# Optimization experiments

Hardware: AMD Instinct MI355X
Metric: run time of the kernel (lower is better)

## Reference

```python
import jax, jax.numpy as jnp
import numpy as np

N = 20000          # num nodes
E = 320000         # num edges
D = 128            # in_channels (= out_channels)
H = 8              # num_heads
HD = D // H        # head_dim = 16


def setup_inputs() -> dict:
    key = jax.random.key(0)
    ks = jax.random.split(key, 10)
    s = 0.05
    return {
        "x": jax.random.normal(ks[0], (N, D), jnp.float32),
        "edges": jax.random.randint(ks[1], (E, 2), 0, N, jnp.int64),
        "Wp": jax.random.normal(ks[2], (D, D), jnp.float32) * s,
        "bp": jax.random.normal(ks[3], (D,), jnp.float32) * s,
        "Wm": jax.random.normal(ks[4], (D, D), jnp.float32) * s,
        "bm": jax.random.normal(ks[5], (D,), jnp.float32) * s,
        "W1": jax.random.normal(ks[6], (D, 2 * D), jnp.float32) * s,
        "b1": jax.random.normal(ks[7], (D,), jnp.float32) * s,
        "W2": jax.random.normal(ks[8], (D, D), jnp.float32) * s,
        "b2": jax.random.normal(ks[9], (D,), jnp.float32) * s,
    }


def reference(x, edges, Wp, bp, Wm, bm, W1, b1, W2, b2):
    # edges: [E,2] -> row (src), col (dst)
    row, col = edges[:, 0], edges[:, 1]
    src = x[row]                       # [E, D] gather
    dst = x[col]                       # [E, D] gather
    # shared preprocess Linear for q, k, v (key == value == dst features)
    q = src @ Wp.T + bp                # [E, D]
    kv = dst @ Wp.T + bp               # [E, D]
    # view(E, -1, H, HD).transpose(1,2) with seq_len 1 -> effectively [E, H, HD]
    q = q.reshape(E, H, HD)
    k = kv.reshape(E, H, HD)
    v = k
    # original attention() misreads axes: contracts over HEAD axis, scale 1/sqrt(H),
    # softmax over the head_dim axis -> scores [E, HD, HD]
    scores = jnp.einsum("ehn,ehm->enm", q, k) / jnp.sqrt(jnp.float32(H))
    prob = jax.nn.softmax(scores, axis=-1)          # [E, HD, HD]
    out = jnp.einsum("enm,ehm->ehn", prob, v)       # [E, H, HD]
    # view(E, HD*H, 1) then 1x1 Conv1d merge == Linear
    msg = out.reshape(E, H * HD) @ Wm.T + bm        # [E, D]
    # scatter-sum aggregate by destination node (empty -> 0, matches torch loop)
    agg = jax.ops.segment_sum(msg, col, num_segments=N)  # [N, D]
    h = jnp.concatenate([x, agg], axis=1)           # [N, 2D]
    h = jax.nn.relu(h @ W1.T + b1)
    return h @ W2.T + b2                            # [N, D]
```

## Files before the change

kernel.cpp:

```cpp
#include <hip/hip_runtime.h>

#define NN 20000
#define EE 320000
#define DEGCAP 64

typedef _Float16 half4_t __attribute__((ext_vector_type(4)));
typedef float f32x4 __attribute__((ext_vector_type(4)));

#define MFMA16F16 __builtin_amdgcn_mfma_f32_16x16x16f16

__global__ __launch_bounds__(256) void setup_kernel(
    int4* __restrict__ countv,
    const float* __restrict__ Wp, const float* __restrict__ Wm,
    const float* __restrict__ W1, const float* __restrict__ W2,
    _Float16* __restrict__ wpt, _Float16* __restrict__ wmt,
    _Float16* __restrict__ w1t, _Float16* __restrict__ w2t) {
  const int b = blockIdx.x, t = threadIdx.x;
  if (b < 20) {
    countv[b * 256 + t] = int4{0, 0, 0, 0};
    return;
  }
  const int tid = (b - 20) * 256 + t;
  const float* W; _Float16* dst; int K, l;
  if (tid < 16384)      { W = Wp; dst = wpt; K = 128; l = tid; }
  else if (tid < 32768) { W = Wm; dst = wmt; K = 128; l = tid - 16384; }
  else if (tid < 65536) { W = W1; dst = w1t; K = 256; l = tid - 32768; }
  else                  { W = W2; dst = w2t; K = 128; l = tid - 65536; }
  const int j = l & 3, n = (l >> 2) & 15, g = (l >> 6) & 3;
  const int ot = (l >> 8) & 7, kt = l >> 11;
  const int k = kt * 16 + 4 * g + j, o = ot * 16 + n;
  dst[l] = (_Float16)W[o * K + k];
}

__global__ __launch_bounds__(256) void bin_proj_kernel(
    const int* __restrict__ edges, int* __restrict__ count,
    int* __restrict__ srow,
    const float* __restrict__ x, const _Float16* __restrict__ wpt,
    const float* __restrict__ bp, _Float16* __restrict__ ph) {
  const int b = blockIdx.x, t = threadIdx.x;
  if (b < 1250) {
    const int e = b * 256 + t;
    const int row = edges[2 * e];
    const int col = edges[2 * e + 1];
    const int slot = atomicAdd(&count[col], 1);
    if (slot < DEGCAP) srow[col * DEGCAP + slot] = row;
    return;
  }
  const int wv = __builtin_amdgcn_readfirstlane(t >> 6), lane = t & 63;
  const int n = lane & 15, g = lane >> 4;
  const int rb = (b - 1250) * 16;
  const int arow = rb + n;

  half4_t a[8];
#pragma unroll
  for (int kt = 0; kt < 8; ++kt) {
    const float4 xv = *(const float4*)&x[(size_t)arow * 128 + kt * 16 + 4 * g];
    half4_t h; h[0] = (_Float16)xv.x; h[1] = (_Float16)xv.y;
    h[2] = (_Float16)xv.z; h[3] = (_Float16)xv.w;
    a[kt] = h;
  }
  const f32x4 zero = {0.f, 0.f, 0.f, 0.f};
#pragma unroll
  for (int oi = 0; oi < 2; ++oi) {
    const int ot = wv * 2 + oi;
    f32x4 acc = zero;
#pragma unroll
    for (int kt = 0; kt < 8; ++kt) {
      const half4_t bb = *(const half4_t*)&wpt[(((kt * 8 + ot) * 4 + g) << 6) + n * 4];
      acc = MFMA16F16(a[kt], bb, acc, 0, 0, 0);
    }
    const float bpv = bp[ot * 16 + n];
#pragma unroll
    for (int r = 0; r < 4; ++r) {
      const int nrow = rb + 4 * g + r;
      ph[(size_t)nrow * 128 + n * 8 + ot] = (_Float16)(acc[r] + bpv);
    }
  }
}

__global__ __launch_bounds__(512) void edge_node_kernel(
    const _Float16* __restrict__ ph, const int* __restrict__ count,
    const int* __restrict__ srow,
    const float* __restrict__ x,
    const _Float16* __restrict__ wmt, const float* __restrict__ bm,
    const _Float16* __restrict__ w1t, const float* __restrict__ b1,
    const _Float16* __restrict__ w2t, const float* __restrict__ b2,
    float* __restrict__ out) {
  __shared__ _Float16 agl[16 * 132];
  __shared__ _Float16 mh[16 * 132];
  __shared__ _Float16 hh[16 * 132];
  const int t = threadIdx.x;
  const int wv = __builtin_amdgcn_readfirstlane(t >> 6);
  const int lane = t & 63;
  const int n = lane & 15, g = lane >> 4;
  const int rb = blockIdx.x * 16;
  const f32x4 zero = {0.f, 0.f, 0.f, 0.f};
  const float c2 = 0.5101268320290106f;
  const int laneoff = n * 8 + 4 * g;

  const int col0 = rb + wv * 2, col1 = col0 + 1;
  const _Float16* __restrict__ pc0 = ph + ((unsigned)col0 << 7);
  const _Float16* __restrict__ pc1 = ph + ((unsigned)col1 << 7);
  half4_t ka0{}, ka1{};
  if (g < 2) {
    ka0 = *(const half4_t*)&pc0[n * 8 + 4 * g];
    ka1 = *(const half4_t*)&pc1[n * 8 + 4 * g];
  }
  half4_t a20{}, a21{};
  if (n < 8) {
#pragma unroll
    for (int j = 0; j < 4; ++j) {
      a20[j] = pc0[(4 * g + j) * 8 + n];
      a21[j] = pc1[(4 * g + j) * 8 + n];
    }
  }
  const int d0raw = count[col0], d1raw = count[col1];
  const int deg0 = (d0raw < DEGCAP) ? d0raw : DEGCAP;
  const int deg1 = (d1raw < DEGCAP) ? d1raw : DEGCAP;
  const int dm0 = (deg0 > 0) ? deg0 - 1 : 0;
  const int dm1 = (deg1 > 0) ? deg1 - 1 : 0;
  const int maxdeg = (deg0 > deg1) ? deg0 : deg1;
  const int slots0 = srow[col0 * DEGCAP + lane];
  const int slots1 = srow[col1 * DEGCAP + lane];
  f32x4 psum0 = zero, psum1 = zero;

#define GATHER(DST, SLOTS, DM, IDX)                                          \
  {                                                                          \
    const int ii_ = ((IDX) < (DM)) ? (IDX) : (DM);                           \
    int row_ = __builtin_amdgcn_readlane(SLOTS, ii_);                        \
    row_ = ((unsigned)row_ < NN) ? row_ : 0;        \
    DST = *(const half4_t*)&ph[((unsigned)row_ << 7) + laneoff];             \
  }
#define PROC(Q, KA, PSUM, IDX, DEG)                                          \
  {                                                                          \
    f32x4 s_ = MFMA16F16(KA, Q, zero, 0, 0, 0);                              \
    const float p0_ = __builtin_amdgcn_exp2f((float)s_[0] * c2);             \
    const float p1_ = __builtin_amdgcn_exp2f((float)s_[1] * c2);             \
    const float p2_ = __builtin_amdgcn_exp2f((float)s_[2] * c2);             \
    const float p3_ = __builtin_amdgcn_exp2f((float)s_[3] * c2);             \
    float sum_ = (p0_ + p1_) + (p2_ + p3_);                                  \
    sum_ += __shfl_xor(sum_, 16, 64);                                        \
    sum_ += __shfl_xor(sum_, 32, 64);                                        \
    const float inv_ =                                                       \
        ((IDX) < (DEG)) ? __builtin_amdgcn_rcpf(sum_) : 0.f;                 \
    PSUM[0] = fmaf(p0_, inv_, PSUM[0]);                                      \
    PSUM[1] = fmaf(p1_, inv_, PSUM[1]);                                      \
    PSUM[2] = fmaf(p2_, inv_, PSUM[2]);                                      \
    PSUM[3] = fmaf(p3_, inv_, PSUM[3]);                                      \
  }

  if (maxdeg > 0) {
    half4_t qA0, qA1, qB0, qB1;
    GATHER(qA0, slots0, dm0, 0) GATHER(qB0, slots1, dm1, 0)
    GATHER(qA1, slots0, dm0, 1) GATHER(qB1, slots1, dm1, 1)
    int i = 0;
    for (; i + 2 <= maxdeg; i += 2) {
      PROC(qA0, ka0, psum0, i, deg0)     GATHER(qA0, slots0, dm0, i + 2)
      PROC(qB0, ka1, psum1, i, deg1)     GATHER(qB0, slots1, dm1, i + 2)
      PROC(qA1, ka0, psum0, i + 1, deg0) GATHER(qA1, slots0, dm0, i + 3)
      PROC(qB1, ka1, psum1, i + 1, deg1) GATHER(qB1, slots1, dm1, i + 3)
    }
    if (i < maxdeg) {
      PROC(qA0, ka0, psum0, i, deg0)
      PROC(qB0, ka1, psum1, i, deg1)
    }
  }
#undef GATHER
#undef PROC

  {
    half4_t pb0, pb1;
#pragma unroll
    for (int r = 0; r < 4; ++r) {
      pb0[r] = (_Float16)psum0[r];
      pb1[r] = (_Float16)psum1[r];
    }
    f32x4 o0 = MFMA16F16(a20, pb0, zero, 0, 0, 0);
    f32x4 o1 = MFMA16F16(a21, pb1, zero, 0, 0, 0);
    if (g < 2) {
#pragma unroll
      for (int r = 0; r < 4; ++r) {
        agl[(wv * 2) * 132 + (4 * g + r) * 16 + n] = (_Float16)o0[r];
        agl[(wv * 2 + 1) * 132 + (4 * g + r) * 16 + n] = (_Float16)o1[r];
      }
    }
  }

  float cnt_r[4];
#pragma unroll
  for (int r = 0; r < 4; ++r)
    cnt_r[r] = (float)count[rb + 4 * g + r];

  __syncthreads();

  const int ot = wv;
  half4_t am[8];
#pragma unroll
  for (int kt = 0; kt < 8; ++kt)
    am[kt] = *(const half4_t*)&agl[n * 132 + kt * 16 + 4 * g];
  {
    f32x4 acc = zero;
#pragma unroll
    for (int kt = 0; kt < 8; ++kt) {
      const half4_t b = *(const half4_t*)&wmt[(((kt * 8 + ot) * 4 + g) << 6) + n * 4];
      acc = MFMA16F16(am[kt], b, acc, 0, 0, 0);
    }
    const float bmv = bm[ot * 16 + n];
#pragma unroll
    for (int r = 0; r < 4; ++r)
      mh[(4 * g + r) * 132 + ot * 16 + n] = (_Float16)(acc[r] + cnt_r[r] * bmv);
  }

  half4_t ah[16];
#pragma unroll
  for (int kt = 0; kt < 8; ++kt) {
    const float4 xv = *(const float4*)&x[(size_t)(rb + n) * 128 + kt * 16 + 4 * g];
    half4_t h; h[0] = (_Float16)xv.x; h[1] = (_Float16)xv.y;
    h[2] = (_Float16)xv.z; h[3] = (_Float16)xv.w;
    ah[kt] = h;
  }
  __syncthreads();
#pragma unroll
  for (int kt = 0; kt < 8; ++kt)
    ah[8 + kt] = *(const half4_t*)&mh[n * 132 + kt * 16 + 4 * g];
  {
    f32x4 acc = zero;
#pragma unroll
    for (int kt = 0; kt < 16; ++kt) {
      const half4_t b = *(const half4_t*)&w1t[(((kt * 8 + ot) * 4 + g) << 6) + n * 4];
      acc = MFMA16F16(ah[kt], b, acc, 0, 0, 0);
    }
    const float b1v = b1[ot * 16 + n];
#pragma unroll
    for (int r = 0; r < 4; ++r)
      hh[(4 * g + r) * 132 + ot * 16 + n] = (_Float16)fmaxf(acc[r] + b1v, 0.f);
  }

  __syncthreads();
  half4_t ay[8];
#pragma unroll
  for (int kt = 0; kt < 8; ++kt)
    ay[kt] = *(const half4_t*)&hh[n * 132 + kt * 16 + 4 * g];
  {
    f32x4 acc = zero;
#pragma unroll
    for (int kt = 0; kt < 8; ++kt) {
      const half4_t b = *(const half4_t*)&w2t[(((kt * 8 + ot) * 4 + g) << 6) + n * 4];
      acc = MFMA16F16(ay[kt], b, acc, 0, 0, 0);
    }
    const float b2v = b2[ot * 16 + n];
#pragma unroll
    for (int r = 0; r < 4; ++r)
      out[(size_t)(rb + 4 * g + r) * 128 + ot * 16 + n] = acc[r] + b2v;
  }
}

extern "C" void kernel_launch(void* const* d_in, const int* in_sizes, int n_in,
                              void* d_out, int out_size, void* d_ws, size_t ws_size,
                              hipStream_t stream) {
  const float* x = (const float*)d_in[0];
  const int* edges = (const int*)d_in[1];
  const float* Wp = (const float*)d_in[2];
  const float* bp = (const float*)d_in[3];
  const float* Wm = (const float*)d_in[4];
  const float* bm = (const float*)d_in[5];
  const float* W1 = (const float*)d_in[6];
  const float* b1 = (const float*)d_in[7];
  const float* W2 = (const float*)d_in[8];
  const float* b2 = (const float*)d_in[9];
  float* out = (float*)d_out;

  _Float16* ph   = (_Float16*)d_ws;
  _Float16* wpt  = ph + (size_t)NN * 128;
  _Float16* wmt  = wpt + 16384;
  _Float16* w1t  = wmt + 16384;
  _Float16* w2t  = w1t + 32768;
  int* count = (int*)(w2t + 16384);
  int* srow  = count + 20480;

  setup_kernel<<<340, 256, 0, stream>>>((int4*)count, Wp, Wm, W1, W2,
                                        wpt, wmt, w1t, w2t);
  bin_proj_kernel<<<2500, 256, 0, stream>>>(edges, count, srow,
                                            x, wpt, bp, ph);
  edge_node_kernel<<<NN / 16, 512, 0, stream>>>(ph, count, srow, x,
                                                wmt, bm, w1t, b1, w2t, b2, out);
}
```

Measured before the change: 78.74 us.

## Use 32x32x16 MFMA to process both destination nodes per edge step

```diff
diff --git a/kernel.cpp b/kernel.cpp
--- a/kernel.cpp
+++ b/kernel.cpp
@@ -5,9 +5,12 @@
 #define DEGCAP 64
 
 typedef _Float16 half4_t __attribute__((ext_vector_type(4)));
+typedef _Float16 half8 __attribute__((ext_vector_type(8)));
 typedef float f32x4 __attribute__((ext_vector_type(4)));
+typedef float f32x16 __attribute__((ext_vector_type(16)));
 
 #define MFMA16F16 __builtin_amdgcn_mfma_f32_16x16x16f16
+#define MFMA32F16 __builtin_amdgcn_mfma_f32_32x32x16_f16
 
 __global__ __launch_bounds__(256) void setup_kernel(
     int4* __restrict__ countv,
@@ -93,96 +96,115 @@
   const int wv = __builtin_amdgcn_readfirstlane(t >> 6);
   const int lane = t & 63;
   const int n = lane & 15, g = lane >> 4;
+  const int r31 = lane & 31;
+  const bool hi = lane >= 32;
+  const bool sel = r31 < 16;
   const int rb = blockIdx.x * 16;
   const f32x4 zero = {0.f, 0.f, 0.f, 0.f};
-  const float c2 = 0.5101268320290106f;
-  const int laneoff = n * 8 + 4 * g;
+  const f32x16 z16 = {};
 
   const int col0 = rb + wv * 2, col1 = col0 + 1;
   const _Float16* __restrict__ pc0 = ph + ((unsigned)col0 << 7);
   const _Float16* __restrict__ pc1 = ph + ((unsigned)col1 << 7);
-  half4_t ka0{}, ka1{};
-  if (g < 2) {
-    ka0 = *(const half4_t*)&pc0[n * 8 + 4 * g];
-    ka1 = *(const half4_t*)&pc1[n * 8 + 4 * g];
-  }
-  half4_t a20{}, a21{};
-  if (n < 8) {
-#pragma unroll
-    for (int j = 0; j < 4; ++j) {
-      a20[j] = pc0[(4 * g + j) * 8 + n];
-      a21[j] = pc1[(4 * g + j) * 8 + n];
-    }
-  }
+  const _Float16* __restrict__ psrc = sel ? pc0 : pc1;
+
+  half8 af{};
+  if (!hi) {
+    af = *(const half8*)&psrc[(r31 & 15) * 8];
+    const _Float16 c2h = (_Float16)0.5101268320290106f;
+#pragma unroll
+    for (int j = 0; j < 8; ++j) af[j] = af[j] * c2h;
+  }
+  half8 a2{};
+  {
+    const int hl = r31 & 15;
+    if (hl < 8) {
+#pragma unroll
+      for (int j = 0; j < 8; ++j) a2[j] = psrc[(8 * (hi ? 1 : 0) + j) * 8 + hl];
+    }
+  }
+
   const int d0raw = count[col0], d1raw = count[col1];
   const int deg0 = (d0raw < DEGCAP) ? d0raw : DEGCAP;
   const int deg1 = (d1raw < DEGCAP) ? d1raw : DEGCAP;
   const int dm0 = (deg0 > 0) ? deg0 - 1 : 0;
   const int dm1 = (deg1 > 0) ? deg1 - 1 : 0;
   const int maxdeg = (deg0 > deg1) ? deg0 : deg1;
+  const int deg_v = sel ? deg0 : deg1;
   const int slots0 = srow[col0 * DEGCAP + lane];
   const int slots1 = srow[col1 * DEGCAP + lane];
-  f32x4 psum0 = zero, psum1 = zero;
-
-#define GATHER(DST, SLOTS, DM, IDX)                                          \
+  const int boff = (lane & 15) * 8;
+
+  float p0 = 0.f, p1 = 0.f, p2 = 0.f, p3 = 0.f;
+  float p4 = 0.f, p5 = 0.f, p6 = 0.f, p7 = 0.f;
+
+#define GATHER(DST, IDX)                                                     \
   {                                                                          \
-    const int ii_ = ((IDX) < (DM)) ? (IDX) : (DM);                           \
-    int row_ = __builtin_amdgcn_readlane(SLOTS, ii_);                        \
-    row_ = ((unsigned)row_ < NN) ? row_ : 0;        \
-    DST = *(const half4_t*)&ph[((unsigned)row_ << 7) + laneoff];             \
-  }
-#define PROC(Q, KA, PSUM, IDX, DEG)                                          \
+    const int i0_ = ((IDX) < dm0) ? (IDX) : dm0;                             \
+    const int i1_ = ((IDX) < dm1) ? (IDX) : dm1;                             \
+    int ra_ = __builtin_amdgcn_readlane(slots0, i0_);                        \
+    int rb_ = __builtin_amdgcn_readlane(slots1, i1_);                        \
+    ra_ = ((unsigned)ra_ < NN) ? ra_ : 0;           \
+    rb_ = ((unsigned)rb_ < NN) ? rb_ : 0;                                    \
+    const int row_ = sel ? ra_ : rb_;                                        \
+    DST = *(const half8*)&ph[((unsigned)row_ << 7) + boff];                  \
+  }
+#define PROC(Q, IDX)                                                         \
   {                                                                          \
-    f32x4 s_ = MFMA16F16(KA, Q, zero, 0, 0, 0);                              \
-    const float p0_ = __builtin_amdgcn_exp2f((float)s_[0] * c2);             \
-    const float p1_ = __builtin_amdgcn_exp2f((float)s_[1] * c2);             \
-    const float p2_ = __builtin_amdgcn_exp2f((float)s_[2] * c2);             \
-    const float p3_ = __builtin_amdgcn_exp2f((float)s_[3] * c2);             \
-    float sum_ = (p0_ + p1_) + (p2_ + p3_);                                  \
-    sum_ += __shfl_xor(sum_, 16, 64);                                        \
+    const f32x16 s_ = MFMA32F16(af, Q, z16, 0, 0, 0);                        \
+    const float e0_ = __builtin_amdgcn_exp2f(sel ? s_[0] : s_[8]);           \
+    const float e1_ = __builtin_amdgcn_exp2f(sel ? s_[1] : s_[9]);           \
+    const float e2_ = __builtin_amdgcn_exp2f(sel ? s_[2] : s_[10]);          \
+    const float e3_ = __builtin_amdgcn_exp2f(sel ? s_[3] : s_[11]);          \
+    const float e4_ = __builtin_amdgcn_exp2f(sel ? s_[4] : s_[12]);          \
+    const float e5_ = __builtin_amdgcn_exp2f(sel ? s_[5] : s_[13]);          \
+    const float e6_ = __builtin_amdgcn_exp2f(sel ? s_[6] : s_[14]);          \
+    const float e7_ = __builtin_amdgcn_exp2f(sel ? s_[7] : s_[15]);          \
+    float sum_ = ((e0_ + e1_) + (e2_ + e3_)) + ((e4_ + e5_) + (e6_ + e7_));  \
     sum_ += __shfl_xor(sum_, 32, 64);                                        \
     const float inv_ =                                                       \
-        ((IDX) < (DEG)) ? __builtin_amdgcn_rcpf(sum_) : 0.f;                 \
-    PSUM[0] = fmaf(p0_, inv_, PSUM[0]);                                      \
-    PSUM[1] = fmaf(p1_, inv_, PSUM[1]);                                      \
-    PSUM[2] = fmaf(p2_, inv_, PSUM[2]);                                      \
-    PSUM[3] = fmaf(p3_, inv_, PSUM[3]);                                      \
+        ((IDX) < deg_v) ? __builtin_amdgcn_rcpf(sum_) : 0.f;                 \
+    p0 = fmaf(e0_, inv_, p0); p1 = fmaf(e1_, inv_, p1);                      \
+    p2 = fmaf(e2_, inv_, p2); p3 = fmaf(e3_, inv_, p3);                      \
+    p4 = fmaf(e4_, inv_, p4); p5 = fmaf(e5_, inv_, p5);                      \
+    p6 = fmaf(e6_, inv_, p6); p7 = fmaf(e7_, inv_, p7);                      \
   }
 
   if (maxdeg > 0) {
-    half4_t qA0, qA1, qB0, qB1;
-    GATHER(qA0, slots0, dm0, 0) GATHER(qB0, slots1, dm1, 0)
-    GATHER(qA1, slots0, dm0, 1) GATHER(qB1, slots1, dm1, 1)
+    half8 q0, q1, q2, q3;
+    GATHER(q0, 0) GATHER(q1, 1) GATHER(q2, 2) GATHER(q3, 3)
     int i = 0;
-    for (; i + 2 <= maxdeg; i += 2) {
-      PROC(qA0, ka0, psum0, i, deg0)     GATHER(qA0, slots0, dm0, i + 2)
-      PROC(qB0, ka1, psum1, i, deg1)     GATHER(qB0, slots1, dm1, i + 2)
-      PROC(qA1, ka0, psum0, i + 1, deg0) GATHER(qA1, slots0, dm0, i + 3)
-      PROC(qB1, ka1, psum1, i + 1, deg1) GATHER(qB1, slots1, dm1, i + 3)
-    }
-    if (i < maxdeg) {
-      PROC(qA0, ka0, psum0, i, deg0)
-      PROC(qB0, ka1, psum1, i, deg1)
-    }
+    for (; i + 4 <= maxdeg; i += 4) {
+      PROC(q0, i)     GATHER(q0, i + 4)
+      PROC(q1, i + 1) GATHER(q1, i + 5)
+      PROC(q2, i + 2) GATHER(q2, i + 6)
+      PROC(q3, i + 3) GATHER(q3, i + 7)
+    }
+    const int rem = maxdeg - i;
+    if (rem > 0) PROC(q0, i)
+    if (rem > 1) PROC(q1, i + 1)
+    if (rem > 2) PROC(q2, i + 2)
   }
 #undef GATHER
 #undef PROC
 
   {
-    half4_t pb0, pb1;
+    const float s0 = __shfl_xor(p0, 32, 64), s1 = __shfl_xor(p1, 32, 64);
+    const float s2 = __shfl_xor(p2, 32, 64), s3 = __shfl_xor(p3, 32, 64);
+    const float s4 = __shfl_xor(p4, 32, 64), s5 = __shfl_xor(p5, 32, 64);
+    const float s6 = __shfl_xor(p6, 32, 64), s7 = __shfl_xor(p7, 32, 64);
+    half8 b2h;
+    b2h[0] = (_Float16)(hi ? s4 : p0); b2h[1] = (_Float16)(hi ? s5 : p1);
+    b2h[2] = (_Float16)(hi ? s6 : p2); b2h[3] = (_Float16)(hi ? s7 : p3);
+    b2h[4] = (_Float16)(hi ? p4 : s0); b2h[5] = (_Float16)(hi ? p5 : s1);
+    b2h[6] = (_Float16)(hi ? p6 : s2); b2h[7] = (_Float16)(hi ? p7 : s3);
+    const f32x16 o = MFMA32F16(a2, b2h, z16, 0, 0, 0);
+    const int lc = wv * 2 + (sel ? 0 : 1);
+    const int hbase = hi ? 4 : 0;
 #pragma unroll
     for (int r = 0; r < 4; ++r) {
-      pb0[r] = (_Float16)psum0[r];
-      pb1[r] = (_Float16)psum1[r];
-    }
-    f32x4 o0 = MFMA16F16(a20, pb0, zero, 0, 0, 0);
-    f32x4 o1 = MFMA16F16(a21, pb1, zero, 0, 0, 0);
-    if (g < 2) {
-#pragma unroll
-      for (int r = 0; r < 4; ++r) {
-        agl[(wv * 2) * 132 + (4 * g + r) * 16 + n] = (_Float16)o0[r];
-        agl[(wv * 2 + 1) * 132 + (4 * g + r) * 16 + n] = (_Float16)o1[r];
-      }
+      const float v = sel ? o[r] : o[8 + r];
+      agl[lc * 132 + (hbase + r) * 16 + n] = (_Float16)v;
     }
   }
 
```

After: 84.89 us. +7.8%, slower.
